# Performance work log

Hardware: AMD Instinct MI355X
Metric: run time of the kernel (lower is better)

The kernel has to match this reference:

```python
import jax, jax.numpy as jnp
import numpy as np
from jax import lax

B, L, V = 64, 48, 50000
E = 300   # emb_dim == repr_dim
F0 = 300  # fc0_dim
F1 = 300  # fc1_dim
NC = 2    # n_classes
NEG = -1e9


def setup_inputs() -> dict:
    key = jax.random.key(0)
    ks = jax.random.split(key, 16)
    inp = {
        "q1": jax.random.randint(ks[0], (B, L), 0, V, dtype=jnp.int64) if jax.config.read('jax_enable_x64') else jax.random.randint(ks[0], (B, L), 0, V, dtype=jnp.int32),
        "q2": jax.random.randint(ks[1], (B, L), 0, V, dtype=jnp.int32),
        "q1_len": jax.random.randint(ks[2], (B,), 1, L + 1, dtype=jnp.int32),
        "q2_len": jax.random.randint(ks[3], (B,), 1, L + 1, dtype=jnp.int32),
        "emb": jax.random.normal(ks[4], (V, E), jnp.float32) * 0.1,
        "conv_w": jax.random.normal(ks[5], (E, E, 3), jnp.float32) * 0.03,
        "conv_b": jnp.zeros((E,), jnp.float32),
        "fc0_w": jax.random.normal(ks[6], (F0, 2 * E), jnp.float32) * 0.04,
        "fc0_b": jnp.zeros((F0,), jnp.float32),
        "fc1_w": jax.random.normal(ks[7], (F1, 2 * F0), jnp.float32) * 0.04,
        "fc1_b": jnp.zeros((F1,), jnp.float32),
        "fc2_w": jax.random.normal(ks[8], (NC, F1), jnp.float32) * 0.05,
        "fc2_b": jnp.zeros((NC,), jnp.float32),
        "att_w": jax.random.normal(ks[9], (1, E + F0), jnp.float32) * 0.05,
        "att_b": jnp.zeros((1,), jnp.float32),
    }
    return inp


def _encode(q, emb, conv_w, conv_b):
    x = emb[q]                                   # [B, L, E]
    x = jnp.transpose(x, (0, 2, 1))              # [B, E, L] (NCW)
    y = lax.conv_general_dilated(x, conv_w, (1,), [(1, 1)],
                                 dimension_numbers=("NCW", "OIW", "NCW"))
    y = jnp.tanh(y + conv_b[None, :, None])
    return jnp.transpose(y, (0, 2, 1))           # [B, L, E]


def reference(q1, q2, q1_len, q2_len, emb, conv_w, conv_b, fc0_w, fc0_b,
              fc1_w, fc1_b, fc2_w, fc2_b, att_w, att_b):
    r1 = _encode(q1, emb, conv_w, conv_b)        # [B, L, E]
    r2 = _encode(q2, emb, conv_w, conv_b)
    pos = jnp.arange(L)
    m1 = pos[None, :] < q1_len[:, None]          # [B, L] valid-token masks
    m2 = pos[None, :] < q2_len[:, None]

    # pairwise features: |r1_i - r2_j| and r1_i * r2_j  -> fc0 -> tanh
    d = jnp.abs(r1[:, :, None, :] - r2[:, None, :, :])   # [B, L1, L2, E]
    p = r1[:, :, None, :] * r2[:, None, :, :]
    Wd, Wp = fc0_w[:, :E], fc0_w[:, E:]
    joint = jnp.tanh(jnp.einsum("bije,fe->bijf", d, Wd)
                     + jnp.einsum("bije,fe->bijf", p, Wp)
                     + fc0_b)                             # [B, L1, L2, F0]

    # masked max-pooling over the other sequence
    s1 = jnp.where(m2[:, None, :, None], joint, NEG).max(axis=2)  # [B, L1, F0]
    s2 = jnp.where(m1[:, :, None, None], joint, NEG).max(axis=1)  # [B, L2, F0]

    # attention-weighted sums (softmax over valid positions only)
    def pool(r, s, m):
        logits = jnp.einsum("bld,d->bl", jnp.concatenate([r, s], -1), att_w[0]) + att_b[0]
        a = jax.nn.softmax(jnp.where(m, logits, NEG), axis=1)     # [B, L]
        return jnp.einsum("bl,blf->bf", a, s)                     # [B, F0]

    h1 = pool(r1, s1, m1)
    h2 = pool(r2, s2, m2)

    j = jnp.tanh(jnp.concatenate([h1, h2], axis=1) @ fc1_w.T + fc1_b)
    return j @ fc2_w.T + fc2_b                                   # [B, 2]
```

## Files before the change

kernel.cpp:

```cpp
#include <hip/hip_runtime.h>
#include <math.h>

#define B_  64
#define L_  48
#define E_  300
#define F0_ 300
#define NEGP (-1e30f)
#define XROW 320
#define RS  312

typedef __attribute__((ext_vector_type(8))) _Float16 half8;
typedef __attribute__((ext_vector_type(8))) short   short8;
typedef __attribute__((ext_vector_type(4))) float   float4v;


__global__ __launch_bounds__(256) void kp_all(
    const int* __restrict__ q1, const int* __restrict__ q2,
    const float* __restrict__ emb, const float* __restrict__ conv_w,
    const float* __restrict__ fc0w,
    _Float16* __restrict__ Bp2, _Float16* __restrict__ Bc,
    _Float16* __restrict__ X)
{
    int u = blockIdx.x * 256 + threadIdx.x;
    if (u < 24320) {
        int m = u >> 8, rest = u & 255;
        int nt = rest >> 6, lane = rest & 63;
        int f = (m / 19) * 64 + nt * 16 + (lane & 15);
        int kb = (m % 19) * 32 + ((lane >> 4) << 3);
        half8 hv;
#pragma unroll
        for (int j = 0; j < 8; ++j) {
            int k = kb + j;
            float v = 0.f;
            if (f < 300) {
                if (k < 300) v = fc0w[f * 600 + k];
                else if (k >= 304 && k < 604) v = fc0w[f * 600 + k - 4];
            }
            hv[j] = (_Float16)v;
        }
        *reinterpret_cast<half8*>(Bp2 + (long)u * 8) = hv;
    } else if (u < 60800) {
        int v = u - 24320;
        int m = v / 1216, rest = v - m * 1216;
        int ntg = rest >> 6, lane = rest & 63;
        int o = ntg * 16 + (lane & 15);
        int kkb = (m % 10) * 32 + ((lane >> 4) << 3);
        int k = m / 10;
        half8 hv;
#pragma unroll
        for (int j = 0; j < 8; ++j) {
            int kk = kkb + j;
            float val = 0.f;
            if (o < 300 && kk < 300) val = conv_w[(o * 300 + kk) * 3 + k];
            hv[j] = (_Float16)val;
        }
        *reinterpret_cast<half8*>(Bc + (long)v * 8) = hv;
    } else if (u < 306560) {
        int v = u - 60800;
        int g = v / 40;
        int e8 = (v - g * 40) * 8;
        int s = g / 3072;
        int rem = g - s * 3072;
        long row = (long)((s ? q2 : q1)[rem]) * 300;
        half8 hv;
        if (e8 + 7 < 300) {
            float4 a = *reinterpret_cast<const float4*>(emb + row + e8);
            float4 c = *reinterpret_cast<const float4*>(emb + row + e8 + 4);
            hv[0] = (_Float16)a.x; hv[1] = (_Float16)a.y; hv[2] = (_Float16)a.z; hv[3] = (_Float16)a.w;
            hv[4] = (_Float16)c.x; hv[5] = (_Float16)c.y; hv[6] = (_Float16)c.z; hv[7] = (_Float16)c.w;
        } else {
#pragma unroll
            for (int j = 0; j < 8; ++j) {
                int i = e8 + j;
                hv[j] = (_Float16)((i < 300) ? emb[row + i] : 0.f);
            }
        }
        *reinterpret_cast<half8*>(X + (long)g * XROW + e8) = hv;
    }
}

__global__ __launch_bounds__(256, 4) void kc_conv(
    const _Float16* __restrict__ X, const _Float16* __restrict__ Bc,
    const float* __restrict__ conv_b, float* __restrict__ r1, float* __restrict__ r2)
{
    int wid = blockIdx.x * 4 + (threadIdx.x >> 6);
    int lane = threadIdx.x & 63;
    int mt = wid / 10;
    int pr = wid - mt * 10;
    int ntg0 = pr * 2;
    bool two = (ntg0 + 1 < 19);
    int row0 = mt * 16;
    int q = lane >> 4, jcol = lane & 15;
    int grow = row0 + jcol;
    int l = grow % 48;

    auto zero8 = []() { half8 z; for (int e = 0; e < 8; ++e) z[e] = (_Float16)0.f; return z; };
    auto loadA = [&](int m) -> half8 {
        int k = m / 10, kk0 = (m - k * 10) * 32;
        int srcl = l + k - 1;
        if (srcl >= 0 && srcl < 48)
            return *reinterpret_cast<const half8*>(X + (long)(grow + k - 1) * XROW + kk0 + q * 8);
        return zero8();
    };
    auto loadB = [&](int m, int ntg) -> half8 {
        return *reinterpret_cast<const half8*>(Bc + ((long)m * 19 + ntg) * 512 + lane * 8);
    };

    float4v acc0 = (float4v){0.f, 0.f, 0.f, 0.f};
    float4v acc1 = (float4v){0.f, 0.f, 0.f, 0.f};

    half8 a_c  = loadA(0);
    half8 b0_c = loadB(0, ntg0);
    half8 b1_c = two ? loadB(0, ntg0 + 1) : b0_c;

    for (int m = 0; m < 30; ++m) {
        half8 a_n, b0_n, b1_n;
        if (m < 29) {
            a_n  = loadA(m + 1);
            b0_n = loadB(m + 1, ntg0);
            b1_n = two ? loadB(m + 1, ntg0 + 1) : b0_n;
        } else { a_n = a_c; b0_n = b0_c; b1_n = b1_c; }
        acc0 = __builtin_amdgcn_mfma_f32_16x16x32_f16(a_c, b0_c, acc0, 0, 0, 0);
        if (two)
            acc1 = __builtin_amdgcn_mfma_f32_16x16x32_f16(a_c, b1_c, acc1, 0, 0, 0);
        a_c = a_n; b0_c = b0_n; b1_c = b1_n;
    }

#pragma unroll
    for (int t = 0; t < 2; ++t) {
        if (t == 1 && !two) break;
        int n = (ntg0 + t) * 16 + jcol;
        if (n >= 300) continue;
        float bias = conv_b[n];
        const float4v& a = t ? acc1 : acc0;
#pragma unroll
        for (int r = 0; r < 4; ++r) {
            int g = row0 + q * 4 + r;
            int s = g / 3072;
            int rem = g - s * 3072;
            float* rout = s ? r2 : r1;
            rout[(long)rem * 300 + n] = tanhf(a[r] + bias);
        }
    }
}

__global__ __launch_bounds__(256, 3) void k2_joint(
    const float* __restrict__ r1, const float* __restrict__ r2,
    const int* __restrict__ q1_len, const int* __restrict__ q2_len,
    const _Float16* __restrict__ Bp2,
    float* __restrict__ s1p, float* __restrict__ s2p)
{
    int x = blockIdx.x;
    int tile = x / 5, nc = x - tile * 5;
    int it = tile / 3, jt = tile - it * 3;
    int b = blockIdx.y;
    int tid = threadIdx.x;
    int q1l = q1_len[b], q2l = q2_len[b];
    long base1 = ((long)(b * 3 + jt) * 48 + it * 16) * 300;
    long base2 = ((long)(b * 3 + it) * 48 + jt * 16) * 300;
    bool active = (it * 16 < q1l) && (jt * 16 < q2l);
    if (!active) {
        for (int idx = tid; idx < 2048; idx += 256) {
            int side = idx >> 10;
            int rest = idx & 1023;
            int row = rest >> 6;
            int f = nc * 64 + (rest & 63);
            if (f < 300) (side ? s2p + base2 : s1p + base1)[row * 300 + f] = NEGP;
        }
        return;
    }

    __shared__ __align__(16) unsigned char smraw[16 * RS * 2 * 2];
    _Float16* r1h = (_Float16*)smraw;
    _Float16* r2h = r1h + 16 * RS;
    float* red = (float*)smraw;

    {
        const float* r1base = r1 + ((long)(b * 48) + it * 16) * 300;
        const float* r2base = r2 + ((long)(b * 48) + jt * 16) * 300;
        for (int u = tid; u < 1200; u += 256) {
            int row = u / 75;
            int e4 = (u - row * 75) * 4;
            float4 v1 = *reinterpret_cast<const float4*>(r1base + row * 300 + e4);
            float4 v2 = *reinterpret_cast<const float4*>(r2base + row * 300 + e4);
            _Float16* d1 = r1h + row * RS + e4;
            _Float16* d2 = r2h + row * RS + e4;
            d1[0] = (_Float16)v1.x; d1[1] = (_Float16)v1.y; d1[2] = (_Float16)v1.z; d1[3] = (_Float16)v1.w;
            d2[0] = (_Float16)v2.x; d2[1] = (_Float16)v2.y; d2[2] = (_Float16)v2.z; d2[3] = (_Float16)v2.w;
        }
        for (int u = tid; u < 2 * 16 * (RS - 300); u += 256) {
            int half = u / (16 * (RS - 300));
            int rest = u - half * 16 * (RS - 300);
            int row = rest / (RS - 300);
            int e = 300 + rest - row * (RS - 300);
            (half ? r2h : r1h)[row * RS + e] = (_Float16)0.f;
        }
    }
    __syncthreads();

    int w    = tid >> 6;
    int lane = tid & 63;
    int q    = lane >> 4;
    int jcol = lane & 15;

    float4v acc[4][4];
#pragma unroll
    for (int mt = 0; mt < 4; ++mt)
#pragma unroll
        for (int nt = 0; nt < 4; ++nt) acc[mt][nt] = (float4v){0.f, 0.f, 0.f, 0.f};

    const _Float16* bbase = Bp2 + (long)(nc * 19) * 2048;
    half8 b0 = *reinterpret_cast<const half8*>(bbase + lane * 8);
    half8 b1 = *reinterpret_cast<const half8*>(bbase + 512 + lane * 8);
    half8 b2 = *reinterpret_cast<const half8*>(bbase + 1024 + lane * 8);
    half8 b3 = *reinterpret_cast<const half8*>(bbase + 1536 + lane * 8);

    for (int kc = 0; kc < 19; ++kc) {
        half8 n0, n1, n2, n3;
        if (kc < 18) {
            const _Float16* nb = bbase + (long)(kc + 1) * 2048;
            n0 = *reinterpret_cast<const half8*>(nb + lane * 8);
            n1 = *reinterpret_cast<const half8*>(nb + 512 + lane * 8);
            n2 = *reinterpret_cast<const half8*>(nb + 1024 + lane * 8);
            n3 = *reinterpret_cast<const half8*>(nb + 1536 + lane * 8);
        } else { n0 = b0; n1 = b1; n2 = b2; n3 = b3; }

        int k0q = kc * 32 + q * 8;
        int koff = (k0q < 304) ? k0q : (k0q - 304);
        const half8 rv2 = *reinterpret_cast<const half8*>(r2h + jcol * RS + koff);
        half8 afr[4];
#pragma unroll
        for (int mt = 0; mt < 4; ++mt) {
            const half8 rv1 = *reinterpret_cast<const half8*>(r1h + (w * 4 + mt) * RS + koff);
            if (k0q < 304) {
                half8 dsub = rv1 - rv2;
                short8 s;
                __builtin_memcpy(&s, &dsub, 16);
                s &= (short)0x7FFF;
                __builtin_memcpy(&afr[mt], &s, 16);
            } else {
                afr[mt] = rv1 * rv2;
            }
        }
#pragma unroll
        for (int mt = 0; mt < 4; ++mt) {
            acc[mt][0] = __builtin_amdgcn_mfma_f32_16x16x32_f16(afr[mt], b0, acc[mt][0], 0, 0, 0);
            acc[mt][1] = __builtin_amdgcn_mfma_f32_16x16x32_f16(afr[mt], b1, acc[mt][1], 0, 0, 0);
            acc[mt][2] = __builtin_amdgcn_mfma_f32_16x16x32_f16(afr[mt], b2, acc[mt][2], 0, 0, 0);
            acc[mt][3] = __builtin_amdgcn_mfma_f32_16x16x32_f16(afr[mt], b3, acc[mt][3], 0, 0, 0);
        }
        b0 = n0; b1 = n1; b2 = n2; b3 = n3;
    }

#pragma unroll
    for (int mt = 0; mt < 4; ++mt) {
        int i_l = w * 4 + mt;
#pragma unroll
        for (int nt = 0; nt < 4; ++nt) {
            float mx = NEGP;
#pragma unroll
            for (int r = 0; r < 4; ++r) {
                int j = q * 4 + r;
                if (jt * 16 + j < q2l) mx = fmaxf(mx, acc[mt][nt][r]);
            }
            mx = fmaxf(mx, __shfl_xor(mx, 16));
            mx = fmaxf(mx, __shfl_xor(mx, 32));
            int f = nc * 64 + nt * 16 + jcol;
            if (q == 0 && f < 300) s1p[base1 + i_l * 300 + f] = mx;
        }
    }

    __syncthreads();
#pragma unroll
    for (int nt = 0; nt < 4; ++nt) {
#pragma unroll
        for (int r = 0; r < 4; ++r) {
            float mx = NEGP;
#pragma unroll
            for (int mt = 0; mt < 4; ++mt) {
                int i = it * 16 + w * 4 + mt;
                if (i < q1l) mx = fmaxf(mx, acc[mt][nt][r]);
            }
            red[((w * 16) + q * 4 + r) * 68 + nt * 16 + jcol] = mx;
        }
    }
    __syncthreads();
    for (int vv = tid; vv < 1024; vv += 256) {
        int j = vv >> 6;
        int fcol = vv & 63;
        float mx = red[j * 68 + fcol];
        mx = fmaxf(mx, red[(16 + j) * 68 + fcol]);
        mx = fmaxf(mx, red[(32 + j) * 68 + fcol]);
        mx = fmaxf(mx, red[(48 + j) * 68 + fcol]);
        int f = nc * 64 + fcol;
        if (f < 300) s2p[base2 + (long)j * 300 + f] = mx;
    }
}

__global__ __launch_bounds__(256) void k3a_comb(
    const float* __restrict__ r1, const float* __restrict__ r2,
    const float* __restrict__ s1p, const float* __restrict__ s2p,
    const float* __restrict__ fc0b,
    const float* __restrict__ att_w, const float* __restrict__ att_b,
    float* __restrict__ sg1, float* __restrict__ sg2,
    float* __restrict__ lg)
{
    int wid = blockIdx.x * 4 + (threadIdx.x >> 6);
    int lane = threadIdx.x & 63;
    int side = wid / 3072;
    int rem = wid - side * 3072;
    int b = rem / 48, l = rem - b * 48;
    const float* sp = (side ? s2p : s1p) + (long)b * 43200 + l * 300;
    const float* r  = (side ? r2 : r1) + (long)rem * 300;
    float* sg = (side ? sg2 : sg1) + (long)rem * 300;

    float lacc = 0.f;
    for (int e = lane; e < 300; e += 64) {
        float mx = fmaxf(fmaxf(sp[e], sp[e + 14400]), sp[e + 28800]);
        float s = tanhf(mx + fc0b[e]);
        sg[e] = s;
        lacc += s * att_w[300 + e] + r[e] * att_w[e];
    }
#pragma unroll
    for (int off = 32; off >= 1; off >>= 1) lacc += __shfl_xor(lacc, off);
    if (lane == 0) lg[wid] = lacc + att_b[0];
}

__global__ __launch_bounds__(64) void k4p_pool(
    const float* __restrict__ sg1, const float* __restrict__ sg2,
    const float* __restrict__ lg,
    const int* __restrict__ q1_len, const int* __restrict__ q2_len,
    float* __restrict__ hcat)
{
    int bid = blockIdx.x;
    int side = bid / 320;
    int rest = bid - side * 320;
    int b = rest / 5, fc = rest - b * 5;
    int lane = threadIdx.x;
    int len = (side ? q2_len : q1_len)[b];
    const float* sg = (side ? sg2 : sg1) + (long)b * 48 * 300;

    float lo = (lane < 48) ? lg[(side * 64 + b) * 48 + lane] : NEGP;
    float ml = (lane < len) ? lo : NEGP;
    float mx = ml;
#pragma unroll
    for (int off = 32; off >= 1; off >>= 1) mx = fmaxf(mx, __shfl_xor(mx, off));
    float ex = (lane < len) ? __expf(lo - mx) : 0.f;
    float sm = ex;
#pragma unroll
    for (int off = 32; off >= 1; off >>= 1) sm += __shfl_xor(sm, off);
    float aLv = ex / sm;

    int f = fc * 60 + lane;
    float acc = 0.f;
    for (int l = 0; l < 48; ++l) {
        float a = __shfl(aLv, l);
        if (f < 300) acc += a * sg[(long)l * 300 + f];
    }
    if (f < 300 && lane < 60)
        hcat[b * 600 + side * 300 + f] = acc;
}

__global__ __launch_bounds__(256) void k5a_fc1(
    const float* __restrict__ hcat, const float* __restrict__ fc1w,
    const float* __restrict__ fc1b, float* __restrict__ jl)
{
    int wid = blockIdx.x * 4 + (threadIdx.x >> 6);
    int lane = threadIdx.x & 63;
    int b = wid / 300;
    int g = wid - b * 300;
    const float* h = hcat + (long)b * 600;
    const float* wrow = fc1w + (long)g * 600;
    float acc = 0.f;
    for (int e = lane; e < 600; e += 64)
        acc += h[e] * wrow[e];
#pragma unroll
    for (int off = 32; off >= 1; off >>= 1) acc += __shfl_xor(acc, off);
    if (lane == 0) jl[b * 300 + g] = tanhf(acc + fc1b[g]);
}

__global__ __launch_bounds__(128) void k5b_fc2(
    const float* __restrict__ jl, const float* __restrict__ fc2w,
    const float* __restrict__ fc2b, float* __restrict__ out)
{
    int b = blockIdx.x;
    int o = threadIdx.x >> 6, lane = threadIdx.x & 63;
    float acc = 0.f;
    for (int g = lane; g < 300; g += 64)
        acc += jl[b * 300 + g] * fc2w[o * 300 + g];
#pragma unroll
    for (int off = 32; off >= 1; off >>= 1) acc += __shfl_xor(acc, off);
    if (lane == 0) out[b * 2 + o] = acc + fc2b[o];
}

extern "C" void kernel_launch(void* const* d_in, const int* in_sizes, int n_in,
                              void* d_out, int out_size, void* d_ws, size_t ws_size,
                              hipStream_t stream)
{
    const int*   q1     = (const int*)d_in[0];
    const int*   q2     = (const int*)d_in[1];
    const int*   q1_len = (const int*)d_in[2];
    const int*   q2_len = (const int*)d_in[3];
    const float* emb    = (const float*)d_in[4];
    const float* conv_w = (const float*)d_in[5];
    const float* conv_b = (const float*)d_in[6];
    const float* fc0_w  = (const float*)d_in[7];
    const float* fc0_b  = (const float*)d_in[8];
    const float* fc1_w  = (const float*)d_in[9];
    const float* fc1_b  = (const float*)d_in[10];
    const float* fc2_w  = (const float*)d_in[11];
    const float* fc2_b  = (const float*)d_in[12];
    const float* att_w  = (const float*)d_in[13];
    const float* att_b  = (const float*)d_in[14];

    float* ws  = (float*)d_ws;
    float* r1  = ws;
    float* r2  = ws + 921600;
    float* s1p = ws + 1843200;
    float* s2p = ws + 4608000;
    float* sg1 = ws + 7372800;
    float* sg2 = ws + 8294400;
    float* hcat = ws + 9216000;
    float* jl   = ws + 9351680;
    float* lg   = ws + 9370880;
    _Float16* X   = (_Float16*)(ws + 1843200);
    _Float16* Bc  = (_Float16*)(ws + 2826240);
    _Float16* Bp2 = (_Float16*)(ws + 9254400);
    float* out = (float*)d_out;

    hipLaunchKernelGGL(kp_all, dim3(1198), dim3(256), 0, stream,
                       q1, q2, emb, conv_w, fc0_w, Bp2, Bc, X);
    hipLaunchKernelGGL(kc_conv, dim3(960), dim3(256), 0, stream,
                       X, Bc, conv_b, r1, r2);
    hipLaunchKernelGGL(k2_joint, dim3(45, 64), dim3(256), 0, stream,
                       r1, r2, q1_len, q2_len, Bp2, s1p, s2p);
    hipLaunchKernelGGL(k3a_comb, dim3(1536), dim3(256), 0, stream,
                       r1, r2, s1p, s2p, fc0_b, att_w, att_b, sg1, sg2, lg);
    hipLaunchKernelGGL(k4p_pool, dim3(640), dim3(64), 0, stream,
                       sg1, sg2, lg, q1_len, q2_len, hcat);
    hipLaunchKernelGGL(k5a_fc1, dim3(4800), dim3(256), 0, stream,
                       hcat, fc1_w, fc1_b, jl);
    hipLaunchKernelGGL(k5b_fc2, dim3(64), dim3(128), 0, stream,
                       jl, fc2_w, fc2_b, out);
}
```

Measured before the change: 217.9 us.

## Emit fp16 padded encoder output from conv and deepen prefetch to two stages

The conv kernel now also writes a half-precision copy of its tanh output, with rows padded to 304 and zeroed tail columns. The joint kernel loads that copy straight into shared memory with 16-byte vector copies, instead of reading fp32 rows and converting them element by element. Both the conv and joint inner loops move from a one-step to a two-step register prefetch of operands. The aim is to cut global read bytes and conversion work in the joint kernel and hide load latency better, at the cost of extra stores in conv and higher register pressure.

```diff
diff --git a/kernel.cpp b/kernel.cpp
--- a/kernel.cpp
+++ b/kernel.cpp
@@ -81,7 +81,8 @@
 
 __global__ __launch_bounds__(256, 4) void kc_conv(
     const _Float16* __restrict__ X, const _Float16* __restrict__ Bc,
-    const float* __restrict__ conv_b, float* __restrict__ r1, float* __restrict__ r2)
+    const float* __restrict__ conv_b, float* __restrict__ r1, float* __restrict__ r2,
+    _Float16* __restrict__ r16)
 {
     int wid = blockIdx.x * 4 + (threadIdx.x >> 6);
     int lane = threadIdx.x & 63;
@@ -109,43 +110,51 @@
     float4v acc0 = (float4v){0.f, 0.f, 0.f, 0.f};
     float4v acc1 = (float4v){0.f, 0.f, 0.f, 0.f};
 
-    half8 a_c  = loadA(0);
-    half8 b0_c = loadB(0, ntg0);
-    half8 b1_c = two ? loadB(0, ntg0 + 1) : b0_c;
+    half8 a0 = loadA(0), p0 = loadB(0, ntg0), s0 = two ? loadB(0, ntg0 + 1) : p0;
+    half8 a1 = loadA(1), p1 = loadB(1, ntg0), s1 = two ? loadB(1, ntg0 + 1) : p1;
 
     for (int m = 0; m < 30; ++m) {
-        half8 a_n, b0_n, b1_n;
-        if (m < 29) {
-            a_n  = loadA(m + 1);
-            b0_n = loadB(m + 1, ntg0);
-            b1_n = two ? loadB(m + 1, ntg0 + 1) : b0_n;
-        } else { a_n = a_c; b0_n = b0_c; b1_n = b1_c; }
-        acc0 = __builtin_amdgcn_mfma_f32_16x16x32_f16(a_c, b0_c, acc0, 0, 0, 0);
+        half8 a2, p2, s2;
+        if (m + 2 < 30) {
+            a2 = loadA(m + 2);
+            p2 = loadB(m + 2, ntg0);
+            s2 = two ? loadB(m + 2, ntg0 + 1) : p2;
+        } else { a2 = a1; p2 = p1; s2 = s1; }
+        acc0 = __builtin_amdgcn_mfma_f32_16x16x32_f16(a0, p0, acc0, 0, 0, 0);
         if (two)
-            acc1 = __builtin_amdgcn_mfma_f32_16x16x32_f16(a_c, b1_c, acc1, 0, 0, 0);
-        a_c = a_n; b0_c = b0_n; b1_c = b1_n;
+            acc1 = __builtin_amdgcn_mfma_f32_16x16x32_f16(a0, s0, acc1, 0, 0, 0);
+        a0 = a1; p0 = p1; s0 = s1;
+        a1 = a2; p1 = p2; s1 = s2;
     }
 
 #pragma unroll
     for (int t = 0; t < 2; ++t) {
         if (t == 1 && !two) break;
         int n = (ntg0 + t) * 16 + jcol;
-        if (n >= 300) continue;
-        float bias = conv_b[n];
         const float4v& a = t ? acc1 : acc0;
-#pragma unroll
-        for (int r = 0; r < 4; ++r) {
-            int g = row0 + q * 4 + r;
-            int s = g / 3072;
-            int rem = g - s * 3072;
-            float* rout = s ? r2 : r1;
-            rout[(long)rem * 300 + n] = tanhf(a[r] + bias);
+        if (n < 300) {
+            float bias = conv_b[n];
+#pragma unroll
+            for (int r = 0; r < 4; ++r) {
+                int g = row0 + q * 4 + r;
+                int s = g / 3072;
+                int rem = g - s * 3072;
+                float val = tanhf(a[r] + bias);
+                (s ? r2 : r1)[(long)rem * 300 + n] = val;
+                r16[(long)g * 304 + n] = (_Float16)val;
+            }
+        } else if (n < 304) {
+#pragma unroll
+            for (int r = 0; r < 4; ++r) {
+                int g = row0 + q * 4 + r;
+                r16[(long)g * 304 + n] = (_Float16)0.f;
+            }
         }
     }
 }
 
 __global__ __launch_bounds__(256, 3) void k2_joint(
-    const float* __restrict__ r1, const float* __restrict__ r2,
+    const _Float16* __restrict__ r16,
     const int* __restrict__ q1_len, const int* __restrict__ q2_len,
     const _Float16* __restrict__ Bp2,
     float* __restrict__ s1p, float* __restrict__ s2p)
@@ -175,26 +184,20 @@
     _Float16* r2h = r1h + 16 * RS;
     float* red = (float*)smraw;
 
+    for (int u = tid; u < 1216; u += 256) {
+        int half_ = u / 608;
+        int rest = u - half_ * 608;
+        int row = rest / 38;
+        int e8 = (rest - row * 38) * 8;
+        long gsrc = (long)(half_ * 3072 + b * 48 + (half_ ? jt : it) * 16 + row);
+        half8 v = *reinterpret_cast<const half8*>(r16 + gsrc * 304 + e8);
+        *reinterpret_cast<half8*>((half_ ? r2h : r1h) + row * RS + e8) = v;
+    }
     {
-        const float* r1base = r1 + ((long)(b * 48) + it * 16) * 300;
-        const float* r2base = r2 + ((long)(b * 48) + jt * 16) * 300;
-        for (int u = tid; u < 1200; u += 256) {
-            int row = u / 75;
-            int e4 = (u - row * 75) * 4;
-            float4 v1 = *reinterpret_cast<const float4*>(r1base + row * 300 + e4);
-            float4 v2 = *reinterpret_cast<const float4*>(r2base + row * 300 + e4);
-            _Float16* d1 = r1h + row * RS + e4;
-            _Float16* d2 = r2h + row * RS + e4;
-            d1[0] = (_Float16)v1.x; d1[1] = (_Float16)v1.y; d1[2] = (_Float16)v1.z; d1[3] = (_Float16)v1.w;
-            d2[0] = (_Float16)v2.x; d2[1] = (_Float16)v2.y; d2[2] = (_Float16)v2.z; d2[3] = (_Float16)v2.w;
-        }
-        for (int u = tid; u < 2 * 16 * (RS - 300); u += 256) {
-            int half = u / (16 * (RS - 300));
-            int rest = u - half * 16 * (RS - 300);
-            int row = rest / (RS - 300);
-            int e = 300 + rest - row * (RS - 300);
-            (half ? r2h : r1h)[row * RS + e] = (_Float16)0.f;
-        }
+        int half_ = tid >> 7;
+        int row = (tid >> 3) & 15;
+        int e = 304 + (tid & 7);
+        (half_ ? r2h : r1h)[row * RS + e] = (_Float16)0.f;
     }
     __syncthreads();
 
@@ -210,20 +213,24 @@
         for (int nt = 0; nt < 4; ++nt) acc[mt][nt] = (float4v){0.f, 0.f, 0.f, 0.f};
 
     const _Float16* bbase = Bp2 + (long)(nc * 19) * 2048;
-    half8 b0 = *reinterpret_cast<const half8*>(bbase + lane * 8);
-    half8 b1 = *reinterpret_cast<const half8*>(bbase + 512 + lane * 8);
-    half8 b2 = *reinterpret_cast<const half8*>(bbase + 1024 + lane * 8);
-    half8 b3 = *reinterpret_cast<const half8*>(bbase + 1536 + lane * 8);
+    half8 c0 = *reinterpret_cast<const half8*>(bbase + lane * 8);
+    half8 c1 = *reinterpret_cast<const half8*>(bbase + 512 + lane * 8);
+    half8 c2 = *reinterpret_cast<const half8*>(bbase + 1024 + lane * 8);
+    half8 c3 = *reinterpret_cast<const half8*>(bbase + 1536 + lane * 8);
+    half8 d0 = *reinterpret_cast<const half8*>(bbase + 2048 + lane * 8);
+    half8 d1 = *reinterpret_cast<const half8*>(bbase + 2560 + lane * 8);
+    half8 d2 = *reinterpret_cast<const half8*>(bbase + 3072 + lane * 8);
+    half8 d3 = *reinterpret_cast<const half8*>(bbase + 3584 + lane * 8);
 
     for (int kc = 0; kc < 19; ++kc) {
-        half8 n0, n1, n2, n3;
-        if (kc < 18) {
-            const _Float16* nb = bbase + (long)(kc + 1) * 2048;
-            n0 = *reinterpret_cast<const half8*>(nb + lane * 8);
-            n1 = *reinterpret_cast<const half8*>(nb + 512 + lane * 8);
-            n2 = *reinterpret_cast<const half8*>(nb + 1024 + lane * 8);
-            n3 = *reinterpret_cast<const half8*>(nb + 1536 + lane * 8);
-        } else { n0 = b0; n1 = b1; n2 = b2; n3 = b3; }
+        half8 e0, e1, e2, e3;
+        if (kc + 2 < 19) {
+            const _Float16* nb = bbase + (long)(kc + 2) * 2048;
+            e0 = *reinterpret_cast<const half8*>(nb + lane * 8);
+            e1 = *reinterpret_cast<const half8*>(nb + 512 + lane * 8);
+            e2 = *reinterpret_cast<const half8*>(nb + 1024 + lane * 8);
+            e3 = *reinterpret_cast<const half8*>(nb + 1536 + lane * 8);
+        } else { e0 = c0; e1 = c1; e2 = c2; e3 = c3; }
 
         int k0q = kc * 32 + q * 8;
         int koff = (k0q < 304) ? k0q : (k0q - 304);
@@ -244,12 +251,13 @@
         }
 #pragma unroll
         for (int mt = 0; mt < 4; ++mt) {
-            acc[mt][0] = __builtin_amdgcn_mfma_f32_16x16x32_f16(afr[mt], b0, acc[mt][0], 0, 0, 0);
-            acc[mt][1] = __builtin_amdgcn_mfma_f32_16x16x32_f16(afr[mt], b1, acc[mt][1], 0, 0, 0);
-            acc[mt][2] = __builtin_amdgcn_mfma_f32_16x16x32_f16(afr[mt], b2, acc[mt][2], 0, 0, 0);
-            acc[mt][3] = __builtin_amdgcn_mfma_f32_16x16x32_f16(afr[mt], b3, acc[mt][3], 0, 0, 0);
-        }
-        b0 = n0; b1 = n1; b2 = n2; b3 = n3;
+            acc[mt][0] = __builtin_amdgcn_mfma_f32_16x16x32_f16(afr[mt], c0, acc[mt][0], 0, 0, 0);
+            acc[mt][1] = __builtin_amdgcn_mfma_f32_16x16x32_f16(afr[mt], c1, acc[mt][1], 0, 0, 0);
+            acc[mt][2] = __builtin_amdgcn_mfma_f32_16x16x32_f16(afr[mt], c2, acc[mt][2], 0, 0, 0);
+            acc[mt][3] = __builtin_amdgcn_mfma_f32_16x16x32_f16(afr[mt], c3, acc[mt][3], 0, 0, 0);
+        }
+        c0 = d0; c1 = d1; c2 = d2; c3 = d3;
+        d0 = e0; d1 = e1; d2 = e2; d3 = e3;
     }
 
 #pragma unroll
@@ -423,6 +431,7 @@
     float* hcat = ws + 9216000;
     float* jl   = ws + 9351680;
     float* lg   = ws + 9370880;
+    _Float16* r16 = (_Float16*)(ws + 9377024);
     _Float16* X   = (_Float16*)(ws + 1843200);
     _Float16* Bc  = (_Float16*)(ws + 2826240);
     _Float16* Bp2 = (_Float16*)(ws + 9254400);
@@ -431,9 +440,9 @@
     hipLaunchKernelGGL(kp_all, dim3(1198), dim3(256), 0, stream,
                        q1, q2, emb, conv_w, fc0_w, Bp2, Bc, X);
     hipLaunchKernelGGL(kc_conv, dim3(960), dim3(256), 0, stream,
-                       X, Bc, conv_b, r1, r2);
+                       X, Bc, conv_b, r1, r2, r16);
     hipLaunchKernelGGL(k2_joint, dim3(45, 64), dim3(256), 0, stream,
-                       r1, r2, q1_len, q2_len, Bp2, s1p, s2p);
+                       r16, q1_len, q2_len, Bp2, s1p, s2p);
     hipLaunchKernelGGL(k3a_comb, dim3(1536), dim3(256), 0, stream,
                        r1, r2, s1p, s2p, fc0_b, att_w, att_b, sg1, sg2, lg);
     hipLaunchKernelGGL(k4p_pool, dim3(640), dim3(64), 0, stream,
```

After: 218.4 us. About the same (+0.2%).
